# Kernel tuning notes

Measured on AMD Instinct MI355X. Metric: run time of the kernel, lower is better.

The kernel has to match this reference:

```python
import jax, jax.numpy as jnp
import numpy as np

B, I, O, M = 128, 2048, 2048, 20


def setup_inputs() -> dict:
    key = jax.random.key(0)
    k1, k2, k3, k4 = jax.random.split(key, 4)
    stdv = 1.0 / np.sqrt(I)
    x = jax.random.normal(k1, (B, I), dtype=jnp.float32)
    weights = jax.random.uniform(k2, (M, O, I), dtype=jnp.float32, minval=-stdv, maxval=stdv)
    biases = jax.random.uniform(k3, (M, O), dtype=jnp.float32, minval=-stdv, maxval=stdv)
    mode_idx = jax.random.randint(k4, (B,), 0, M, dtype=jnp.int64 if jax.config.jax_enable_x64 else jnp.int32)
    return {"x": x, "weights": weights, "biases": biases, "mode_idx": mode_idx}


def reference(x, weights, biases, mode_idx):
    # non-int mode branch of BayesLinearEMP.forward:
    # per-sample weight gather [B, O, I] then batched matvec + gathered bias
    w = weights[mode_idx]            # [B, O, I]
    b = biases[mode_idx]             # [B, O]
    out = jnp.einsum('boi,bi->bo', w, x) + b
    return out
```

## Files before the change

kernel.cpp:

```cpp
#include <hip/hip_runtime.h>


#define M_MODES 20
#define B_SAMP  128
#define I_DIM   2048
#define O_DIM   2048
#define RPW     4
#define ROWS_PER_BLOCK 16
#define OTILES  (O_DIM / ROWS_PER_BLOCK)

typedef float f32x4 __attribute__((ext_vector_type(4)));

__global__ void group_kernel(const int* __restrict__ mode_idx,
                             int* __restrict__ counts,
                             int* __restrict__ lists) {
    __shared__ int cnt[M_MODES];
    const int tid = threadIdx.x;
    if (tid < M_MODES) cnt[tid] = 0;
    __syncthreads();
    if (tid < B_SAMP) {
        const int m = mode_idx[tid];
        const int pos = atomicAdd(&cnt[m], 1);
        lists[m * B_SAMP + pos] = tid;
    }
    __syncthreads();
    if (tid < M_MODES) counts[tid] = cnt[tid];
}

template<int SC, int S0>
__device__ __forceinline__ void fma8(const float* const (&xb)[SC], int i,
                                     const f32x4 (&w4)[RPW],
                                     float (&acc)[RPW][SC]) {
    constexpr int G = (SC - S0) < 8 ? (SC - S0) : 8;
    f32x4 xv[G];
    #pragma unroll
    for (int s = 0; s < G; ++s)
        xv[s] = *reinterpret_cast<const f32x4*>(xb[S0 + s] + i);
    #pragma unroll
    for (int s = 0; s < G; ++s)
        #pragma unroll
        for (int r = 0; r < RPW; ++r)
            acc[r][S0 + s] += w4[r][0] * xv[s][0] + w4[r][1] * xv[s][1]
                            + w4[r][2] * xv[s][2] + w4[r][3] * xv[s][3];
}

template<int SC>
__device__ __forceinline__ void bmv_body(const float* __restrict__ x,
                                         const float* __restrict__ wrow,
                                         const float* __restrict__ biases,
                                         const int*   __restrict__ list,
                                         int scount, int m, int o0, int lane,
                                         float* __restrict__ out) {
    const float* xb[SC];
    #pragma unroll
    for (int s = 0; s < SC; ++s) {
        const int ss  = (s < scount) ? s : (scount - 1);
        int idx = list[ss];
        idx = __builtin_amdgcn_readfirstlane(idx);
        xb[s] = x + (size_t)idx * I_DIM;
    }

    float acc[RPW][SC];
    #pragma unroll
    for (int r = 0; r < RPW; ++r)
        #pragma unroll
        for (int s = 0; s < SC; ++s)
            acc[r][s] = 0.0f;

    for (int i = lane * 4; i < I_DIM; i += 256) {
        f32x4 w4[RPW];
        #pragma unroll
        for (int r = 0; r < RPW; ++r)
            w4[r] = __builtin_nontemporal_load(
                reinterpret_cast<const f32x4*>(wrow + (size_t)r * I_DIM + i));
        fma8<SC, 0>(xb, i, w4, acc);
        if constexpr (SC > 8) fma8<SC, 8>(xb, i, w4, acc);
    }

    constexpr int NV = RPW * SC;
    float v[NV];
    #pragma unroll
    for (int j = 0; j < NV; ++j)
        v[j] = acc[j & (RPW - 1)][j >> 2];
    int D = 32;
    #pragma unroll
    for (int n = NV; n > 1; n >>= 1, D >>= 1) {
        #pragma unroll
        for (int j = 0; j < n / 2; ++j) {
            const float a = v[j], b = v[j + n / 2];
            const bool hi = (lane & D) != 0;
            const float sel = hi ? b : a;
            const float oth = __shfl_xor(hi ? a : b, D, 64);
            v[j] = sel + oth;
        }
    }
    #pragma unroll
    for (int Dr = 64 / NV / 2; Dr >= 1; Dr >>= 1)
        v[0] += __shfl_xor(v[0], Dr, 64);

    constexpr int rep = 64 / NV;
    if ((lane & (rep - 1)) == 0) {
        const int j = lane / rep;
        const int s = j >> 2;
        const int r = j & (RPW - 1);
        if (s < scount) {
            const int idx = list[s];
            out[(size_t)idx * O_DIM + (o0 + r)] =
                v[0] + biases[(size_t)m * O_DIM + o0 + r];
        }
    }
}

__global__ __launch_bounds__(256, 3)
void bmv_kernel(const float* __restrict__ x,
                const float* __restrict__ weights,
                const float* __restrict__ biases,
                const int*   __restrict__ counts,
                const int*   __restrict__ lists,
                float*       __restrict__ out) {
    const int m  = blockIdx.x / OTILES;
    const int ot = blockIdx.x % OTILES;
    const int cnt = counts[m];
    if (cnt == 0) return;

    const int tid  = threadIdx.x;
    const int wv   = tid >> 6;
    const int lane = tid & 63;
    const int o0   = ot * ROWS_PER_BLOCK + wv * RPW;

    const float* wrow = weights + ((size_t)m * O_DIM + o0) * I_DIM;

    for (int s0 = 0; s0 < cnt; s0 += 16) {
        const int sc = min(cnt - s0, 16);
        const int* list = lists + m * B_SAMP + s0;
        if (sc > 8)
            bmv_body<16>(x, wrow, biases, list, sc, m, o0, lane, out);
        else if (sc > 4)
            bmv_body<8>(x, wrow, biases, list, sc, m, o0, lane, out);
        else if (sc > 2)
            bmv_body<4>(x, wrow, biases, list, sc, m, o0, lane, out);
        else if (sc == 2)
            bmv_body<2>(x, wrow, biases, list, sc, m, o0, lane, out);
        else
            bmv_body<1>(x, wrow, biases, list, sc, m, o0, lane, out);
    }
}

extern "C" void kernel_launch(void* const* d_in, const int* in_sizes, int n_in,
                              void* d_out, int out_size, void* d_ws, size_t ws_size,
                              hipStream_t stream) {
    const float* x        = (const float*)d_in[0];
    const float* weights  = (const float*)d_in[1];
    const float* biases   = (const float*)d_in[2];
    const int*   mode_idx = (const int*)d_in[3];
    float* out = (float*)d_out;

    int* counts = (int*)d_ws;
    int* lists  = counts + M_MODES;

    group_kernel<<<1, 128, 0, stream>>>(mode_idx, counts, lists);
    bmv_kernel<<<M_MODES * OTILES, 256, 0, stream>>>(x, weights, biases,
                                                     counts, lists, out);
}
```

Baseline: 81.77 us.

## Fuse mode grouping into matvec kernel and specialize per exact sample count

Drops the separate grouping kernel. Each block now builds its own list of samples for its mode in shared memory using a wave ballot and popcount, which removes one launch and the dependency between the two kernels. It also adds template instantiations closer to the exact sample count, with padding to the next power of two for the reduction, so fewer FLOPs go to duplicated samples. For small counts it loads two chunks of weight rows per iteration to get more memory-level parallelism. The costs are redundant mode_idx reads in every block, extra code size and register pressure from the added instantiations, and the list pointer losing its __restrict__ qualifier.

```diff
diff --git a/kernel.cpp b/kernel.cpp
--- a/kernel.cpp
+++ b/kernel.cpp
@@ -10,22 +10,6 @@
 #define OTILES  (O_DIM / ROWS_PER_BLOCK)
 
 typedef float f32x4 __attribute__((ext_vector_type(4)));
-
-__global__ void group_kernel(const int* __restrict__ mode_idx,
-                             int* __restrict__ counts,
-                             int* __restrict__ lists) {
-    __shared__ int cnt[M_MODES];
-    const int tid = threadIdx.x;
-    if (tid < M_MODES) cnt[tid] = 0;
-    __syncthreads();
-    if (tid < B_SAMP) {
-        const int m = mode_idx[tid];
-        const int pos = atomicAdd(&cnt[m], 1);
-        lists[m * B_SAMP + pos] = tid;
-    }
-    __syncthreads();
-    if (tid < M_MODES) counts[tid] = cnt[tid];
-}
 
 template<int SC, int S0>
 __device__ __forceinline__ void fma8(const float* const (&xb)[SC], int i,
@@ -44,11 +28,17 @@
                             + w4[r][2] * xv[s][2] + w4[r][3] * xv[s][3];
 }
 
+constexpr int next_pow2(int n) {
+    int p = 1;
+    while (p < n) p <<= 1;
+    return p;
+}
+
 template<int SC>
 __device__ __forceinline__ void bmv_body(const float* __restrict__ x,
                                          const float* __restrict__ wrow,
                                          const float* __restrict__ biases,
-                                         const int*   __restrict__ list,
+                                         const int*   list,
                                          int scount, int m, int o0, int lane,
                                          float* __restrict__ out) {
     const float* xb[SC];
@@ -67,24 +57,31 @@
         for (int s = 0; s < SC; ++s)
             acc[r][s] = 0.0f;
 
-    for (int i = lane * 4; i < I_DIM; i += 256) {
-        f32x4 w4[RPW];
+    constexpr int CH = (SC <= 8) ? 2 : 1;
+    for (int i = lane * 4; i < I_DIM; i += 256 * CH) {
+        f32x4 w4[CH][RPW];
         #pragma unroll
-        for (int r = 0; r < RPW; ++r)
-            w4[r] = __builtin_nontemporal_load(
-                reinterpret_cast<const f32x4*>(wrow + (size_t)r * I_DIM + i));
-        fma8<SC, 0>(xb, i, w4, acc);
-        if constexpr (SC > 8) fma8<SC, 8>(xb, i, w4, acc);
+        for (int h = 0; h < CH; ++h)
+            #pragma unroll
+            for (int r = 0; r < RPW; ++r)
+                w4[h][r] = __builtin_nontemporal_load(
+                    reinterpret_cast<const f32x4*>(wrow + (size_t)r * I_DIM + i + h * 256));
+        #pragma unroll
+        for (int h = 0; h < CH; ++h) {
+            fma8<SC, 0>(xb, i + h * 256, w4[h], acc);
+            if constexpr (SC > 8) fma8<SC, 8>(xb, i + h * 256, w4[h], acc);
+        }
     }
 
-    constexpr int NV = RPW * SC;
-    float v[NV];
+    constexpr int NV  = RPW * SC;
+    constexpr int NVP = next_pow2(NV);
+    float v[NVP];
     #pragma unroll
-    for (int j = 0; j < NV; ++j)
-        v[j] = acc[j & (RPW - 1)][j >> 2];
+    for (int j = 0; j < NVP; ++j)
+        v[j] = (j < NV) ? acc[j & (RPW - 1)][j >> 2] : 0.0f;
     int D = 32;
     #pragma unroll
-    for (int n = NV; n > 1; n >>= 1, D >>= 1) {
+    for (int n = NVP; n > 1; n >>= 1, D >>= 1) {
         #pragma unroll
         for (int j = 0; j < n / 2; ++j) {
             const float a = v[j], b = v[j + n / 2];
@@ -95,10 +92,10 @@
         }
     }
     #pragma unroll
-    for (int Dr = 64 / NV / 2; Dr >= 1; Dr >>= 1)
+    for (int Dr = 64 / NVP / 2; Dr >= 1; Dr >>= 1)
         v[0] += __shfl_xor(v[0], Dr, 64);
 
-    constexpr int rep = 64 / NV;
+    constexpr int rep = 64 / NVP;
     if ((lane & (rep - 1)) == 0) {
         const int j = lane / rep;
         const int s = j >> 2;
@@ -115,34 +112,53 @@
 void bmv_kernel(const float* __restrict__ x,
                 const float* __restrict__ weights,
                 const float* __restrict__ biases,
-                const int*   __restrict__ counts,
-                const int*   __restrict__ lists,
+                const int*   __restrict__ mode_idx,
                 float*       __restrict__ out) {
     const int m  = blockIdx.x / OTILES;
     const int ot = blockIdx.x % OTILES;
-    const int cnt = counts[m];
-    if (cnt == 0) return;
 
     const int tid  = threadIdx.x;
     const int wv   = tid >> 6;
     const int lane = tid & 63;
+
+    __shared__ int s_list[B_SAMP];
+    __shared__ int s_wcnt[2];
+    int match = 0, prefix = 0;
+    if (tid < B_SAMP) {
+        match  = (mode_idx[tid] == m);
+        const unsigned long long mask = __ballot(match);
+        prefix = __popcll(mask & ((1ull << lane) - 1));
+        if (lane == 0) s_wcnt[wv] = __popcll(mask);
+    }
+    __syncthreads();
+    const int cnt = s_wcnt[0] + s_wcnt[1];
+    if (match) s_list[prefix + (wv ? s_wcnt[0] : 0)] = tid;
+    __syncthreads();
+    if (cnt == 0) return;
+
     const int o0   = ot * ROWS_PER_BLOCK + wv * RPW;
-
     const float* wrow = weights + ((size_t)m * O_DIM + o0) * I_DIM;
 
     for (int s0 = 0; s0 < cnt; s0 += 16) {
         const int sc = min(cnt - s0, 16);
-        const int* list = lists + m * B_SAMP + s0;
-        if (sc > 8)
-            bmv_body<16>(x, wrow, biases, list, sc, m, o0, lane, out);
-        else if (sc > 4)
-            bmv_body<8>(x, wrow, biases, list, sc, m, o0, lane, out);
-        else if (sc > 2)
-            bmv_body<4>(x, wrow, biases, list, sc, m, o0, lane, out);
-        else if (sc == 2)
-            bmv_body<2>(x, wrow, biases, list, sc, m, o0, lane, out);
-        else
-            bmv_body<1>(x, wrow, biases, list, sc, m, o0, lane, out);
+        const int* list = s_list + s0;
+        switch (sc) {
+            case 1:  bmv_body<1> (x, wrow, biases, list, sc, m, o0, lane, out); break;
+            case 2:  bmv_body<2> (x, wrow, biases, list, sc, m, o0, lane, out); break;
+            case 3:  bmv_body<3> (x, wrow, biases, list, sc, m, o0, lane, out); break;
+            case 4:  bmv_body<4> (x, wrow, biases, list, sc, m, o0, lane, out); break;
+            case 5:  bmv_body<5> (x, wrow, biases, list, sc, m, o0, lane, out); break;
+            case 6:  bmv_body<6> (x, wrow, biases, list, sc, m, o0, lane, out); break;
+            case 7:  bmv_body<7> (x, wrow, biases, list, sc, m, o0, lane, out); break;
+            case 8:  bmv_body<8> (x, wrow, biases, list, sc, m, o0, lane, out); break;
+            case 9:
+            case 10: bmv_body<10>(x, wrow, biases, list, sc, m, o0, lane, out); break;
+            case 11:
+            case 12: bmv_body<12>(x, wrow, biases, list, sc, m, o0, lane, out); break;
+            case 13:
+            case 14: bmv_body<14>(x, wrow, biases, list, sc, m, o0, lane, out); break;
+            default: bmv_body<16>(x, wrow, biases, list, sc, m, o0, lane, out); break;
+        }
     }
 }
 
@@ -155,10 +171,6 @@
     const int*   mode_idx = (const int*)d_in[3];
     float* out = (float*)d_out;
 
-    int* counts = (int*)d_ws;
-    int* lists  = counts + M_MODES;
-
-    group_kernel<<<1, 128, 0, stream>>>(mode_idx, counts, lists);
     bmv_kernel<<<M_MODES * OTILES, 256, 0, stream>>>(x, weights, biases,
-                                                     counts, lists, out);
+                                                     mode_idx, out);
 }
```

Result: slower. 84.01 us (+2.7%).
